# Optimization experiments

Measured on AMD Instinct MI355X. Metric: run time of the kernel, lower is better.

The kernel has to match this reference:

```python
import jax, jax.numpy as jnp
import numpy as np

B, N, D, K = 4, 256, 128, 8
H = 2 * D   # MLP hidden
F3 = 3 * D  # pair feature dim


def setup_inputs() -> dict:
    key = jax.random.key(0)
    ks = jax.random.split(key, 9)
    init = lambda k, shape: (jax.random.normal(k, shape, jnp.float32) * 0.02)
    s = jax.random.normal(ks[0], (B, N, D), jnp.float32)
    return {
        "s": s,
        "Wg1": init(ks[1], (F3, H)), "bg1": jnp.zeros((H,), jnp.float32),
        "Wg2": init(ks[2], (H, 1)),  "bg2": jnp.zeros((1,), jnp.float32),
        "Wa1": init(ks[3], (F3, H)), "ba1": jnp.zeros((H,), jnp.float32),
        "Wa2": init(ks[4], (H, 1)),  "ba2": jnp.zeros((1,), jnp.float32),
    }


def _mlp(x, W1, b1, W2, b2):
    # 2-layer MLP: Linear -> ReLU -> Linear (dropout inactive at eval)
    return jax.nn.relu(x @ W1 + b1) @ W2 + b2


def reference(s, Wg1, bg1, Wg2, bg2, Wa1, ba1, Wa2, ba2):
    b, n, d = s.shape
    si = s[:, :, None, :]                      # [B,N,1,D]
    sj = s[:, None, :, :]                      # [B,1,N,D]
    pair = jnp.concatenate([
        jnp.broadcast_to(si, (b, n, n, d)),
        jnp.broadcast_to(sj, (b, n, n, d)),
        si * sj,
    ], axis=-1)                                # [B,N,N,3D]

    # Stage 1: discrete top-K peer gating
    scores = _mlp(pair, Wg1, bg1, Wg2, bg2)[..., 0]   # [B,N,N]
    k = min(K, n)
    _, topk_idx = jax.lax.top_k(scores, k)            # [B,N,K]
    gate = jax.nn.one_hot(topk_idx, n, dtype=jnp.float32).sum(-2)  # [B,N,N] binary

    # Stage 2: soft relevance weighting over selected peers
    att_logits = _mlp(pair, Wa1, ba1, Wa2, ba2)[..., 0]            # [B,N,N]
    att_logits = jnp.where(gate > 0, att_logits, -jnp.inf)
    att_weights = jnp.nan_to_num(jax.nn.softmax(att_logits, axis=-1))

    ctx = jnp.einsum('bij,bij,bjd->bid', gate, att_weights, s)     # [B,N,D]
    return ctx, gate, att_weights
```

## Files before the change

### kernel.cpp

```cpp
#include <hip/hip_runtime.h>
#include <math.h>

#define B_ 4
#define N_ 256
#define D_ 128
#define H_ 256
#define K_ 8
#define KK 256
#define NJP 64

typedef short v8s __attribute__((ext_vector_type(8)));
typedef float v16f __attribute__((ext_vector_type(16)));

__device__ inline void split_bf16(float x, unsigned short& hi, unsigned short& lo) {
  unsigned u = __float_as_uint(x);
  unsigned uh = u & 0xFFFF0000u;
  hi = (unsigned short)(uh >> 16);
  float r = x - __uint_as_float(uh);
  unsigned ur = __float_as_uint(r);
  ur += 0x7FFFu + ((ur >> 16) & 1u);
  lo = (unsigned short)(ur >> 16);
}

__global__ __launch_bounds__(256) void prep_an(
    const float* __restrict__ s,
    const float* __restrict__ Wg1, const float* __restrict__ bg1,
    const float* __restrict__ Wa1, const float* __restrict__ ba1,
    float* __restrict__ Ag, float* __restrict__ Aa,
    unsigned short* __restrict__ Shi, unsigned short* __restrict__ Slo) {
  const int b = blockIdx.x >> 8;
  const int n = blockIdx.x & 255;
  const int h = threadIdx.x;
  __shared__ float sh[D_];
  if (h < D_) sh[h] = s[(b * N_ + n) * D_ + h];
  __syncthreads();
  float ag = bg1[h], aa = ba1[h];
#pragma unroll 8
  for (int d = 0; d < D_; d++) {
    ag = fmaf(sh[d], Wg1[d * H_ + h], ag);
    aa = fmaf(sh[d], Wa1[d * H_ + h], aa);
  }
  Ag[(b * N_ + n) * H_ + h] = ag;
  Aa[(b * N_ + n) * H_ + h] = aa;
  if (h < D_) {
    unsigned short x, y;
    split_bf16(sh[h], x, y);
    Shi[(b * N_ + n) * D_ + h] = x;
    Slo[(b * N_ + n) * D_ + h] = y;
  }
}

__global__ __launch_bounds__(64) void prep_sw(
    const float* __restrict__ Wg1, const float* __restrict__ Wa1,
    unsigned short* __restrict__ Wghi, unsigned short* __restrict__ Wglo,
    unsigned short* __restrict__ Wahi) {
  const int ks = blockIdx.x >> 3;
  const int tile = blockIdx.x & 7;
  const int lane = threadIdx.x;
  const int h = tile * 32 + (lane & 31);
  const int kbase = ks * 16 + (lane >> 5) * 8;
  const int idx0 = (blockIdx.x * 64 + lane) * 8;
#pragma unroll
  for (int e = 0; e < 8; e++) {
    const int k = kbase + e;
    const int f = (k < D_) ? (2 * D_ + k) : k;
    unsigned short x, y;
    split_bf16(Wg1[f * H_ + h], x, y);
    Wghi[idx0 + e] = x;
    Wglo[idx0 + e] = y;
    unsigned short xa, ya;
    split_bf16(Wa1[f * H_ + h], xa, ya);
    Wahi[idx0 + e] = xa;
  }
}

__global__ __launch_bounds__(256) void prep_sf(
    const unsigned short* __restrict__ Shi, const unsigned short* __restrict__ Slo,
    unsigned short* __restrict__ Sfh, unsigned short* __restrict__ Sfl) {
  const int b = blockIdx.x >> 3, jt = blockIdx.x & 7;
  const int lane = threadIdx.x & 63;
  const int k0 = threadIdx.x >> 6;
  const int j = jt * 32 + (lane & 31);
#pragma unroll
  for (int ksl = k0; ksl < 8; ksl += 4) {
    const int d = ksl * 16 + (lane >> 5) * 8;
    const int src = (b * N_ + j) * D_ + d;
    const int dst = (((b * 8 + jt) * 8 + ksl) * 64 + lane) * 8;
    *(v8s*)(Sfh + dst) = *(const v8s*)(Shi + src);
    *(v8s*)(Sfl + dst) = *(const v8s*)(Slo + src);
  }
}

__device__ inline void arg_better(float v2, int i2, float& v, int& idx) {
  if (v2 > v || (v2 == v && i2 < idx)) { v = v2; idx = i2; }
}

__device__ inline int a_idx(int jl, int k) {
  return (((jl >> 5) * 8 + (k >> 4)) * 64 + ((k >> 3) & 1) * 32 + (jl & 31)) * 8
         + (k & 7);
}
#define ALO 8192

__global__ __launch_bounds__(256, 2) void score_kernel(
    const float* __restrict__ s,
    const float* __restrict__ Ag, const float* __restrict__ Aa,
    const unsigned short* __restrict__ Shi, const unsigned short* __restrict__ Slo,
    const unsigned short* __restrict__ Sfh, const unsigned short* __restrict__ Sfl,
    const unsigned short* __restrict__ Wghi, const unsigned short* __restrict__ Wglo,
    const unsigned short* __restrict__ Wahi,
    const float* __restrict__ Wg2, const float* __restrict__ bg2p,
    const float* __restrict__ Wa2, const float* __restrict__ ba2p,
    float* __restrict__ out) {
  const int b = blockIdx.x >> 8;
  const int i = blockIdx.x & 255;
  const int t = threadIdx.x;
  const int wv = t >> 6, lane = t & 63;
  const int m32 = lane & 31, half32 = lane >> 5;

  __shared__ __align__(16) unsigned short a_all[2 * 8192 + 64];
  __shared__ float si_sh[D_];
  __shared__ float sc_part[8 * NJP];
  __shared__ float scg_sh[N_];
  __shared__ float attl_sh[N_];
  __shared__ float red_v[4];
  __shared__ int red_i[4];
  __shared__ int sel_list[K_];

  if (t < D_) si_sh[t] = s[(b * N_ + i) * D_ + t];

  float agv[2], w2g[2], aav[2], w2a[2];
#pragma unroll
  for (int ht = 0; ht < 2; ht++) {
    const int hg = wv * 64 + ht * 32 + m32;
    agv[ht] = Ag[(b * N_ + i) * H_ + hg];
    w2g[ht] = Wg2[hg];
    aav[ht] = Aa[(b * N_ + i) * H_ + hg];
    w2a[ht] = Wa2[hg];
  }

  const int boff = ((2 * wv) * 64 + lane) * 8;

#pragma unroll 1
  for (int ph = 0; ph < 4; ph++) {
    __syncthreads();
    {
      const int jl = t >> 2, kq = t & 3;
      const int jg = b * N_ + ph * NJP + jl;
      const float* srow = s + jg * D_ + kq * 32;
      const float* sic = si_sh + kq * 32;
#pragma unroll
      for (int u = 0; u < 4; u++) {
        const float4 sv0 = *(const float4*)(srow + u * 8);
        const float4 sv1 = *(const float4*)(srow + u * 8 + 4);
        unsigned short hh[8], ll[8];
        split_bf16(sic[u * 8 + 0] * sv0.x, hh[0], ll[0]);
        split_bf16(sic[u * 8 + 1] * sv0.y, hh[1], ll[1]);
        split_bf16(sic[u * 8 + 2] * sv0.z, hh[2], ll[2]);
        split_bf16(sic[u * 8 + 3] * sv0.w, hh[3], ll[3]);
        split_bf16(sic[u * 8 + 4] * sv1.x, hh[4], ll[4]);
        split_bf16(sic[u * 8 + 5] * sv1.y, hh[5], ll[5]);
        split_bf16(sic[u * 8 + 6] * sv1.z, hh[6], ll[6]);
        split_bf16(sic[u * 8 + 7] * sv1.w, hh[7], ll[7]);
        v8s vh, vl;
#pragma unroll
        for (int e = 0; e < 8; e++) { vh[e] = (short)hh[e]; vl[e] = (short)ll[e]; }
        const int idx = a_idx(jl, kq * 32 + u * 8);
        *(v8s*)(a_all + idx) = vh;
        *(v8s*)(a_all + ALO + idx) = vl;
      }
    }
    __syncthreads();

    const unsigned short* sf_base_h = Sfh + ((b * 8 + ph * 2) * 8) * 512 + lane * 8;
    const unsigned short* sf_base_l = Sfl + ((b * 8 + ph * 2) * 8) * 512 + lane * 8;

    {
      v16f acc[2][2];
#pragma unroll
      for (int jt = 0; jt < 2; jt++)
#pragma unroll
        for (int ht = 0; ht < 2; ht++) acc[jt][ht] = (v16f)(0.f);

      const unsigned short* pgh = Wghi + boff;
      const unsigned short* pgl = Wglo + boff;
      v8s bh[2][2], bl[2][2];
      bh[0][0] = *(const v8s*)pgh;  bh[0][1] = *(const v8s*)(pgh + 512);
      bl[0][0] = *(const v8s*)pgl;  bl[0][1] = *(const v8s*)(pgl + 512);
      pgh += 4096;  pgl += 4096;

      const unsigned short* ahp = a_all + lane * 8;
#pragma unroll 2
      for (int ks = 0; ks < 8; ks++) {
        const int cur = ks & 1, nxt = cur ^ 1;
        bh[nxt][0] = *(const v8s*)pgh;  bh[nxt][1] = *(const v8s*)(pgh + 512);
        bl[nxt][0] = *(const v8s*)pgl;  bl[nxt][1] = *(const v8s*)(pgl + 512);
        pgh += 4096;  pgl += 4096;
        v8s ah0 = *(const v8s*)(ahp);
        v8s ah1 = *(const v8s*)(ahp + 4096);
        v8s al0 = *(const v8s*)(ahp + ALO);
        v8s al1 = *(const v8s*)(ahp + ALO + 4096);
        ahp += 512;
        acc[0][0] = __builtin_amdgcn_mfma_f32_32x32x16_bf16(ah0, bh[cur][0], acc[0][0], 0, 0, 0);
        acc[0][1] = __builtin_amdgcn_mfma_f32_32x32x16_bf16(ah0, bh[cur][1], acc[0][1], 0, 0, 0);
        acc[0][0] = __builtin_amdgcn_mfma_f32_32x32x16_bf16(ah0, bl[cur][0], acc[0][0], 0, 0, 0);
        acc[0][1] = __builtin_amdgcn_mfma_f32_32x32x16_bf16(ah0, bl[cur][1], acc[0][1], 0, 0, 0);
        acc[0][0] = __builtin_amdgcn_mfma_f32_32x32x16_bf16(al0, bh[cur][0], acc[0][0], 0, 0, 0);
        acc[0][1] = __builtin_amdgcn_mfma_f32_32x32x16_bf16(al0, bh[cur][1], acc[0][1], 0, 0, 0);
        acc[1][0] = __builtin_amdgcn_mfma_f32_32x32x16_bf16(ah1, bh[cur][0], acc[1][0], 0, 0, 0);
        acc[1][1] = __builtin_amdgcn_mfma_f32_32x32x16_bf16(ah1, bh[cur][1], acc[1][1], 0, 0, 0);
        acc[1][0] = __builtin_amdgcn_mfma_f32_32x32x16_bf16(ah1, bl[cur][0], acc[1][0], 0, 0, 0);
        acc[1][1] = __builtin_amdgcn_mfma_f32_32x32x16_bf16(ah1, bl[cur][1], acc[1][1], 0, 0, 0);
        acc[1][0] = __builtin_amdgcn_mfma_f32_32x32x16_bf16(al1, bh[cur][0], acc[1][0], 0, 0, 0);
        acc[1][1] = __builtin_amdgcn_mfma_f32_32x32x16_bf16(al1, bh[cur][1], acc[1][1], 0, 0, 0);
      }
      const unsigned short* sfh = sf_base_h;
      const unsigned short* sfl = sf_base_l;
#pragma unroll 2
      for (int ks = 8; ks < 16; ks++) {
        const int cur = ks & 1, nxt = cur ^ 1;
        bh[nxt][0] = *(const v8s*)pgh;  bh[nxt][1] = *(const v8s*)(pgh + 512);
        bl[nxt][0] = *(const v8s*)pgl;  bl[nxt][1] = *(const v8s*)(pgl + 512);
        pgh += 4096;  pgl += 4096;
        v8s ah0 = *(const v8s*)(sfh);
        v8s ah1 = *(const v8s*)(sfh + 4096);
        v8s al0 = *(const v8s*)(sfl);
        v8s al1 = *(const v8s*)(sfl + 4096);
        sfh += 512;  sfl += 512;
        acc[0][0] = __builtin_amdgcn_mfma_f32_32x32x16_bf16(ah0, bh[cur][0], acc[0][0], 0, 0, 0);
        acc[0][1] = __builtin_amdgcn_mfma_f32_32x32x16_bf16(ah0, bh[cur][1], acc[0][1], 0, 0, 0);
        acc[0][0] = __builtin_amdgcn_mfma_f32_32x32x16_bf16(ah0, bl[cur][0], acc[0][0], 0, 0, 0);
        acc[0][1] = __builtin_amdgcn_mfma_f32_32x32x16_bf16(ah0, bl[cur][1], acc[0][1], 0, 0, 0);
        acc[0][0] = __builtin_amdgcn_mfma_f32_32x32x16_bf16(al0, bh[cur][0], acc[0][0], 0, 0, 0);
        acc[0][1] = __builtin_amdgcn_mfma_f32_32x32x16_bf16(al0, bh[cur][1], acc[0][1], 0, 0, 0);
        acc[1][0] = __builtin_amdgcn_mfma_f32_32x32x16_bf16(ah1, bh[cur][0], acc[1][0], 0, 0, 0);
        acc[1][1] = __builtin_amdgcn_mfma_f32_32x32x16_bf16(ah1, bh[cur][1], acc[1][1], 0, 0, 0);
        acc[1][0] = __builtin_amdgcn_mfma_f32_32x32x16_bf16(ah1, bl[cur][0], acc[1][0], 0, 0, 0);
        acc[1][1] = __builtin_amdgcn_mfma_f32_32x32x16_bf16(ah1, bl[cur][1], acc[1][1], 0, 0, 0);
        acc[1][0] = __builtin_amdgcn_mfma_f32_32x32x16_bf16(al1, bh[cur][0], acc[1][0], 0, 0, 0);
        acc[1][1] = __builtin_amdgcn_mfma_f32_32x32x16_bf16(al1, bh[cur][1], acc[1][1], 0, 0, 0);
      }
      float sg[32];
#pragma unroll
      for (int m = 0; m < 32; m++) sg[m] = 0.f;
#pragma unroll
      for (int ht = 0; ht < 2; ht++)
#pragma unroll
        for (int jt = 0; jt < 2; jt++)
#pragma unroll
          for (int r = 0; r < 16; r++) {
            const float z = acc[jt][ht][r] + agv[ht];
            sg[jt * 16 + r] = fmaf(fmaxf(z, 0.f), w2g[ht], sg[jt * 16 + r]);
          }
#pragma unroll
      for (int m = 0; m < 32; m++) {
        float v = sg[m];
#pragma unroll
        for (int off = 1; off <= 16; off <<= 1) v += __shfl_xor(v, off, 64);
        sg[m] = v;
      }
      if (m32 == 0) {
#pragma unroll
        for (int jt = 0; jt < 2; jt++)
#pragma unroll
          for (int r = 0; r < 16; r++) {
            const int jl = jt * 32 + (r & 3) + 8 * (r >> 2) + 4 * half32;
            sc_part[wv * NJP + jl] = sg[jt * 16 + r];
          }
      }
    }

    {
      v16f acc[2][2];
#pragma unroll
      for (int jt = 0; jt < 2; jt++)
#pragma unroll
        for (int ht = 0; ht < 2; ht++) acc[jt][ht] = (v16f)(0.f);

      const unsigned short* pah = Wahi + boff;
      v8s bh[2][2];
      bh[0][0] = *(const v8s*)pah;  bh[0][1] = *(const v8s*)(pah + 512);
      pah += 4096;

      const unsigned short* ahp = a_all + lane * 8;
#pragma unroll 2
      for (int ks = 0; ks < 8; ks++) {
        const int cur = ks & 1, nxt = cur ^ 1;
        bh[nxt][0] = *(const v8s*)pah;  bh[nxt][1] = *(const v8s*)(pah + 512);
        pah += 4096;
        v8s ah0 = *(const v8s*)(ahp);
        v8s ah1 = *(const v8s*)(ahp + 4096);
        ahp += 512;
        acc[0][0] = __builtin_amdgcn_mfma_f32_32x32x16_bf16(ah0, bh[cur][0], acc[0][0], 0, 0, 0);
        acc[0][1] = __builtin_amdgcn_mfma_f32_32x32x16_bf16(ah0, bh[cur][1], acc[0][1], 0, 0, 0);
        acc[1][0] = __builtin_amdgcn_mfma_f32_32x32x16_bf16(ah1, bh[cur][0], acc[1][0], 0, 0, 0);
        acc[1][1] = __builtin_amdgcn_mfma_f32_32x32x16_bf16(ah1, bh[cur][1], acc[1][1], 0, 0, 0);
      }
      const unsigned short* sfh = sf_base_h;
#pragma unroll 2
      for (int ks = 8; ks < 16; ks++) {
        const int cur = ks & 1, nxt = cur ^ 1;
        bh[nxt][0] = *(const v8s*)pah;  bh[nxt][1] = *(const v8s*)(pah + 512);
        pah += 4096;
        v8s ah0 = *(const v8s*)(sfh);
        v8s ah1 = *(const v8s*)(sfh + 4096);
        sfh += 512;
        acc[0][0] = __builtin_amdgcn_mfma_f32_32x32x16_bf16(ah0, bh[cur][0], acc[0][0], 0, 0, 0);
        acc[0][1] = __builtin_amdgcn_mfma_f32_32x32x16_bf16(ah0, bh[cur][1], acc[0][1], 0, 0, 0);
        acc[1][0] = __builtin_amdgcn_mfma_f32_32x32x16_bf16(ah1, bh[cur][0], acc[1][0], 0, 0, 0);
        acc[1][1] = __builtin_amdgcn_mfma_f32_32x32x16_bf16(ah1, bh[cur][1], acc[1][1], 0, 0, 0);
      }
      float sa[32];
#pragma unroll
      for (int m = 0; m < 32; m++) sa[m] = 0.f;
#pragma unroll
      for (int ht = 0; ht < 2; ht++)
#pragma unroll
        for (int jt = 0; jt < 2; jt++)
#pragma unroll
          for (int r = 0; r < 16; r++) {
            const float z = acc[jt][ht][r] + aav[ht];
            sa[jt * 16 + r] = fmaf(fmaxf(z, 0.f), w2a[ht], sa[jt * 16 + r]);
          }
#pragma unroll
      for (int m = 0; m < 32; m++) {
        float v = sa[m];
#pragma unroll
        for (int off = 1; off <= 16; off <<= 1) v += __shfl_xor(v, off, 64);
        sa[m] = v;
      }
      if (m32 == 0) {
#pragma unroll
        for (int jt = 0; jt < 2; jt++)
#pragma unroll
          for (int r = 0; r < 16; r++) {
            const int jl = jt * 32 + (r & 3) + 8 * (r >> 2) + 4 * half32;
            sc_part[4 * NJP + wv * NJP + jl] = sa[jt * 16 + r];
          }
      }
    }
    __syncthreads();
    if (t < NJP) {
      scg_sh[ph * NJP + t] = sc_part[t] + sc_part[NJP + t] + sc_part[2 * NJP + t]
                           + sc_part[3 * NJP + t] + bg2p[0];
      attl_sh[ph * NJP + t] = sc_part[4 * NJP + t] + sc_part[5 * NJP + t]
                            + sc_part[6 * NJP + t] + sc_part[7 * NJP + t] + ba2p[0];
    }
  }
  __syncthreads();

  for (int k = 0; k < K_; k++) {
    float v = scg_sh[t];
    int idx = t;
#pragma unroll
    for (int off = 32; off > 0; off >>= 1) {
      const float vo = __shfl_down(v, off, 64);
      const int io = __shfl_down(idx, off, 64);
      arg_better(vo, io, v, idx);
    }
    if ((t & 63) == 0) { red_v[t >> 6] = v; red_i[t >> 6] = idx; }
    __syncthreads();
    if (t == 0) {
      float bv = red_v[0];
      int bi = red_i[0];
      for (int w = 1; w < 4; w++) arg_better(red_v[w], red_i[w], bv, bi);
      sel_list[k] = bi;
      scg_sh[bi] = -INFINITY;
    }
    __syncthreads();
  }

  bool selj = false;
#pragma unroll
  for (int k = 0; k < K_; k++) selj = selj || (sel_list[k] == t);

  if (t == 0) {
    float m = -INFINITY;
    for (int k = 0; k < K_; k++) m = fmaxf(m, attl_sh[sel_list[k]]);
    float ssum = 0.f;
    for (int k = 0; k < K_; k++) ssum += expf(attl_sh[sel_list[k]] - m);
    red_v[0] = m;
    red_v[1] = ssum;
  }
  __syncthreads();
  const float att = selj ? expf(attl_sh[t] - red_v[0]) / red_v[1] : 0.f;

  float* __restrict__ ctx_out = out;
  float* __restrict__ gate_out = out + B_ * N_ * D_;
  float* __restrict__ att_out = out + B_ * N_ * D_ + B_ * N_ * N_;

  const int row = (b * N_ + i) * N_;
  gate_out[row + t] = selj ? 1.f : 0.f;
  att_out[row + t] = att;

  __syncthreads();
  attl_sh[t] = att;
  __syncthreads();

  if (t < D_) {
    float acc2 = 0.f;
#pragma unroll
    for (int k = 0; k < K_; k++) {
      const int jj = sel_list[k];
      acc2 = fmaf(attl_sh[jj], s[(b * N_ + jj) * D_ + t], acc2);
    }
    ctx_out[(b * N_ + i) * D_ + t] = acc2;
  }
}

extern "C" void kernel_launch(void* const* d_in, const int* in_sizes, int n_in,
                              void* d_out, int out_size, void* d_ws, size_t ws_size,
                              hipStream_t stream) {
  const float* s   = (const float*)d_in[0];
  const float* Wg1 = (const float*)d_in[1];
  const float* bg1 = (const float*)d_in[2];
  const float* Wg2 = (const float*)d_in[3];
  const float* bg2 = (const float*)d_in[4];
  const float* Wa1 = (const float*)d_in[5];
  const float* ba1 = (const float*)d_in[6];
  const float* Wa2 = (const float*)d_in[7];
  const float* ba2 = (const float*)d_in[8];
  float* out = (float*)d_out;

  float* ws = (float*)d_ws;
  float* Ag = ws;
  float* Aa = Ag + B_ * N_ * H_;
  unsigned short* Shi  = (unsigned short*)(Aa + B_ * N_ * H_);
  unsigned short* Slo  = Shi + B_ * N_ * D_;
  unsigned short* Wghi = Slo + B_ * N_ * D_;
  unsigned short* Wglo = Wghi + 65536 + 4096;
  unsigned short* Wahi = Wglo + 65536 + 4096;
  unsigned short* Sfh  = Wahi + 65536 + 4096;
  unsigned short* Sfl  = Sfh + B_ * 32768;

  prep_an<<<dim3(B_ * N_), dim3(256), 0, stream>>>(
      s, Wg1, bg1, Wa1, ba1, Ag, Aa, Shi, Slo);
  prep_sw<<<dim3(128), dim3(64), 0, stream>>>(Wg1, Wa1, Wghi, Wglo, Wahi);
  prep_sf<<<dim3(B_ * 8), dim3(256), 0, stream>>>(Shi, Slo, Sfh, Sfl);
  score_kernel<<<dim3(B_ * N_), dim3(256), 0, stream>>>(
      s, Ag, Aa, Shi, Slo, Sfh, Sfl, Wghi, Wglo, Wahi, Wg2, bg2, Wa2, ba2, out);
}
```

Measured before the change: 264.5 us.

## Merge prep kernels into one launch and fuse gate/attention MFMA loops

Combines the three preprocessing kernels into a single launch that branches on block index, and builds the fragment-layout split of s directly from fp32, which drops the intermediate Shi/Slo buffers. In the score kernel, the gating and attention first-layer GEMMs now share one loop, so the A fragments (LDS tile and Sf global loads) are read once and feed both weight sets. This cuts launch overhead and duplicate operand traffic, but holds eight accumulators live at once, which raises register pressure and may hurt occupancy under the 2-blocks launch bound.

```diff
diff --git a/kernel.cpp b/kernel.cpp
--- a/kernel.cpp
+++ b/kernel.cpp
@@ -6,7 +6,6 @@
 #define D_ 128
 #define H_ 256
 #define K_ 8
-#define KK 256
 #define NJP 64
 
 typedef short v8s __attribute__((ext_vector_type(8)));
@@ -22,72 +21,73 @@
   lo = (unsigned short)(ur >> 16);
 }
 
-__global__ __launch_bounds__(256) void prep_an(
+__global__ __launch_bounds__(256) void prep_all(
     const float* __restrict__ s,
     const float* __restrict__ Wg1, const float* __restrict__ bg1,
     const float* __restrict__ Wa1, const float* __restrict__ ba1,
     float* __restrict__ Ag, float* __restrict__ Aa,
-    unsigned short* __restrict__ Shi, unsigned short* __restrict__ Slo) {
-  const int b = blockIdx.x >> 8;
-  const int n = blockIdx.x & 255;
-  const int h = threadIdx.x;
+    unsigned short* __restrict__ Wghi, unsigned short* __restrict__ Wglo,
+    unsigned short* __restrict__ Wahi,
+    unsigned short* __restrict__ Sfh, unsigned short* __restrict__ Sfl) {
   __shared__ float sh[D_];
-  if (h < D_) sh[h] = s[(b * N_ + n) * D_ + h];
-  __syncthreads();
-  float ag = bg1[h], aa = ba1[h];
+  const int blk = blockIdx.x;
+  if (blk < 1024) {
+    const int b = blk >> 8, n = blk & 255, h = threadIdx.x;
+    if (h < D_) sh[h] = s[(b * N_ + n) * D_ + h];
+    __syncthreads();
+    float ag = bg1[h], aa = ba1[h];
 #pragma unroll 8
-  for (int d = 0; d < D_; d++) {
-    ag = fmaf(sh[d], Wg1[d * H_ + h], ag);
-    aa = fmaf(sh[d], Wa1[d * H_ + h], aa);
-  }
-  Ag[(b * N_ + n) * H_ + h] = ag;
-  Aa[(b * N_ + n) * H_ + h] = aa;
-  if (h < D_) {
-    unsigned short x, y;
-    split_bf16(sh[h], x, y);
-    Shi[(b * N_ + n) * D_ + h] = x;
-    Slo[(b * N_ + n) * D_ + h] = y;
-  }
-}
-
-__global__ __launch_bounds__(64) void prep_sw(
-    const float* __restrict__ Wg1, const float* __restrict__ Wa1,
-    unsigned short* __restrict__ Wghi, unsigned short* __restrict__ Wglo,
-    unsigned short* __restrict__ Wahi) {
-  const int ks = blockIdx.x >> 3;
-  const int tile = blockIdx.x & 7;
-  const int lane = threadIdx.x;
-  const int h = tile * 32 + (lane & 31);
-  const int kbase = ks * 16 + (lane >> 5) * 8;
-  const int idx0 = (blockIdx.x * 64 + lane) * 8;
-#pragma unroll
-  for (int e = 0; e < 8; e++) {
-    const int k = kbase + e;
-    const int f = (k < D_) ? (2 * D_ + k) : k;
-    unsigned short x, y;
-    split_bf16(Wg1[f * H_ + h], x, y);
-    Wghi[idx0 + e] = x;
-    Wglo[idx0 + e] = y;
-    unsigned short xa, ya;
-    split_bf16(Wa1[f * H_ + h], xa, ya);
-    Wahi[idx0 + e] = xa;
-  }
-}
-
-__global__ __launch_bounds__(256) void prep_sf(
-    const unsigned short* __restrict__ Shi, const unsigned short* __restrict__ Slo,
-    unsigned short* __restrict__ Sfh, unsigned short* __restrict__ Sfl) {
-  const int b = blockIdx.x >> 3, jt = blockIdx.x & 7;
-  const int lane = threadIdx.x & 63;
-  const int k0 = threadIdx.x >> 6;
-  const int j = jt * 32 + (lane & 31);
-#pragma unroll
-  for (int ksl = k0; ksl < 8; ksl += 4) {
-    const int d = ksl * 16 + (lane >> 5) * 8;
-    const int src = (b * N_ + j) * D_ + d;
-    const int dst = (((b * 8 + jt) * 8 + ksl) * 64 + lane) * 8;
-    *(v8s*)(Sfh + dst) = *(const v8s*)(Shi + src);
-    *(v8s*)(Sfl + dst) = *(const v8s*)(Slo + src);
+    for (int d = 0; d < D_; d++) {
+      ag = fmaf(sh[d], Wg1[d * H_ + h], ag);
+      aa = fmaf(sh[d], Wa1[d * H_ + h], aa);
+    }
+    Ag[(b * N_ + n) * H_ + h] = ag;
+    Aa[(b * N_ + n) * H_ + h] = aa;
+  } else if (blk < 1152) {
+    const int id = blk - 1024;
+    if (threadIdx.x < 64) {
+      const int ks = id >> 3, tile = id & 7, lane = threadIdx.x;
+      const int h = tile * 32 + (lane & 31);
+      const int kbase = ks * 16 + (lane >> 5) * 8;
+      const int idx0 = (id * 64 + lane) * 8;
+#pragma unroll
+      for (int e = 0; e < 8; e++) {
+        const int k = kbase + e;
+        const int f = (k < D_) ? (2 * D_ + k) : k;
+        unsigned short x, y;
+        split_bf16(Wg1[f * H_ + h], x, y);
+        Wghi[idx0 + e] = x;
+        Wglo[idx0 + e] = y;
+        unsigned short xa, ya;
+        split_bf16(Wa1[f * H_ + h], xa, ya);
+        Wahi[idx0 + e] = xa;
+      }
+    }
+  } else {
+    const int id = blk - 1152;
+    const int b = id >> 3, jt = id & 7;
+    const int lane = threadIdx.x & 63, k0 = threadIdx.x >> 6;
+    const int j = jt * 32 + (lane & 31);
+#pragma unroll
+    for (int ksl = k0; ksl < 8; ksl += 4) {
+      const int d = ksl * 16 + (lane >> 5) * 8;
+      const float* sp = s + (b * N_ + j) * D_ + d;
+      const float4 f0 = *(const float4*)(sp);
+      const float4 f1 = *(const float4*)(sp + 4);
+      v8s vh, vl;
+      unsigned short x, y;
+      split_bf16(f0.x, x, y); vh[0] = (short)x; vl[0] = (short)y;
+      split_bf16(f0.y, x, y); vh[1] = (short)x; vl[1] = (short)y;
+      split_bf16(f0.z, x, y); vh[2] = (short)x; vl[2] = (short)y;
+      split_bf16(f0.w, x, y); vh[3] = (short)x; vl[3] = (short)y;
+      split_bf16(f1.x, x, y); vh[4] = (short)x; vl[4] = (short)y;
+      split_bf16(f1.y, x, y); vh[5] = (short)x; vl[5] = (short)y;
+      split_bf16(f1.z, x, y); vh[6] = (short)x; vl[6] = (short)y;
+      split_bf16(f1.w, x, y); vh[7] = (short)x; vl[7] = (short)y;
+      const int dst = (((b * 8 + jt) * 8 + ksl) * 64 + lane) * 8;
+      *(v8s*)(Sfh + dst) = vh;
+      *(v8s*)(Sfl + dst) = vl;
+    }
   }
 }
 
@@ -104,7 +104,6 @@
 __global__ __launch_bounds__(256, 2) void score_kernel(
     const float* __restrict__ s,
     const float* __restrict__ Ag, const float* __restrict__ Aa,
-    const unsigned short* __restrict__ Shi, const unsigned short* __restrict__ Slo,
     const unsigned short* __restrict__ Sfh, const unsigned short* __restrict__ Sfl,
     const unsigned short* __restrict__ Wghi, const unsigned short* __restrict__ Wglo,
     const unsigned short* __restrict__ Wahi,
@@ -117,7 +116,7 @@
   const int wv = t >> 6, lane = t & 63;
   const int m32 = lane & 31, half32 = lane >> 5;
 
-  __shared__ __align__(16) unsigned short a_all[2 * 8192 + 64];
+  __shared__ __align__(16) unsigned short a_all[2 * ALO + 64];
   __shared__ float si_sh[D_];
   __shared__ float sc_part[8 * NJP];
   __shared__ float scg_sh[N_];
@@ -140,6 +139,8 @@
 
   const int boff = ((2 * wv) * 64 + lane) * 8;
 
+#define MF(A_, B_v, C_) C_ = __builtin_amdgcn_mfma_f32_32x32x16_bf16(A_, B_v, C_, 0, 0, 0)
+
 #pragma unroll 1
   for (int ph = 0; ph < 4; ph++) {
     __syncthreads();
@@ -152,18 +153,16 @@
       for (int u = 0; u < 4; u++) {
         const float4 sv0 = *(const float4*)(srow + u * 8);
         const float4 sv1 = *(const float4*)(srow + u * 8 + 4);
-        unsigned short hh[8], ll[8];
-        split_bf16(sic[u * 8 + 0] * sv0.x, hh[0], ll[0]);
-        split_bf16(sic[u * 8 + 1] * sv0.y, hh[1], ll[1]);
-        split_bf16(sic[u * 8 + 2] * sv0.z, hh[2], ll[2]);
-        split_bf16(sic[u * 8 + 3] * sv0.w, hh[3], ll[3]);
-        split_bf16(sic[u * 8 + 4] * sv1.x, hh[4], ll[4]);
-        split_bf16(sic[u * 8 + 5] * sv1.y, hh[5], ll[5]);
-        split_bf16(sic[u * 8 + 6] * sv1.z, hh[6], ll[6]);
-        split_bf16(sic[u * 8 + 7] * sv1.w, hh[7], ll[7]);
         v8s vh, vl;
-#pragma unroll
-        for (int e = 0; e < 8; e++) { vh[e] = (short)hh[e]; vl[e] = (short)ll[e]; }
+        unsigned short x, y;
+        split_bf16(sic[u * 8 + 0] * sv0.x, x, y); vh[0] = (short)x; vl[0] = (short)y;
+        split_bf16(sic[u * 8 + 1] * sv0.y, x, y); vh[1] = (short)x; vl[1] = (short)y;
+        split_bf16(sic[u * 8 + 2] * sv0.z, x, y); vh[2] = (short)x; vl[2] = (short)y;
+        split_bf16(sic[u * 8 + 3] * sv0.w, x, y); vh[3] = (short)x; vl[3] = (short)y;
+        split_bf16(sic[u * 8 + 4] * sv1.x, x, y); vh[4] = (short)x; vl[4] = (short)y;
+        split_bf16(sic[u * 8 + 5] * sv1.y, x, y); vh[5] = (short)x; vl[5] = (short)y;
+        split_bf16(sic[u * 8 + 6] * sv1.z, x, y); vh[6] = (short)x; vl[6] = (short)y;
+        split_bf16(sic[u * 8 + 7] * sv1.w, x, y); vh[7] = (short)x; vl[7] = (short)y;
         const int idx = a_idx(jl, kq * 32 + u * 8);
         *(v8s*)(a_all + idx) = vh;
         *(v8s*)(a_all + ALO + idx) = vl;
@@ -174,19 +173,19 @@
     const unsigned short* sf_base_h = Sfh + ((b * 8 + ph * 2) * 8) * 512 + lane * 8;
     const unsigned short* sf_base_l = Sfl + ((b * 8 + ph * 2) * 8) * 512 + lane * 8;
 
+    v16f g00, g01, g10, g11, a00, a01, a10, a11;
+    g00 = g01 = g10 = g11 = (v16f)(0.f);
+    a00 = a01 = a10 = a11 = (v16f)(0.f);
+
     {
-      v16f acc[2][2];
-#pragma unroll
-      for (int jt = 0; jt < 2; jt++)
-#pragma unroll
-        for (int ht = 0; ht < 2; ht++) acc[jt][ht] = (v16f)(0.f);
-
       const unsigned short* pgh = Wghi + boff;
       const unsigned short* pgl = Wglo + boff;
-      v8s bh[2][2], bl[2][2];
+      const unsigned short* pah = Wahi + boff;
+      v8s bh[2][2], bl[2][2], ba[2][2];
       bh[0][0] = *(const v8s*)pgh;  bh[0][1] = *(const v8s*)(pgh + 512);
       bl[0][0] = *(const v8s*)pgl;  bl[0][1] = *(const v8s*)(pgl + 512);
-      pgh += 4096;  pgl += 4096;
+      ba[0][0] = *(const v8s*)pah;  ba[0][1] = *(const v8s*)(pah + 512);
+      pgh += 4096;  pgl += 4096;  pah += 4096;
 
       const unsigned short* ahp = a_all + lane * 8;
 #pragma unroll 2
@@ -194,24 +193,21 @@
         const int cur = ks & 1, nxt = cur ^ 1;
         bh[nxt][0] = *(const v8s*)pgh;  bh[nxt][1] = *(const v8s*)(pgh + 512);
         bl[nxt][0] = *(const v8s*)pgl;  bl[nxt][1] = *(const v8s*)(pgl + 512);
-        pgh += 4096;  pgl += 4096;
+        ba[nxt][0] = *(const v8s*)pah;  ba[nxt][1] = *(const v8s*)(pah + 512);
+        pgh += 4096;  pgl += 4096;  pah += 4096;
         v8s ah0 = *(const v8s*)(ahp);
         v8s ah1 = *(const v8s*)(ahp + 4096);
         v8s al0 = *(const v8s*)(ahp + ALO);
         v8s al1 = *(const v8s*)(ahp + ALO + 4096);
         ahp += 512;
-        acc[0][0] = __builtin_amdgcn_mfma_f32_32x32x16_bf16(ah0, bh[cur][0], acc[0][0], 0, 0, 0);
-        acc[0][1] = __builtin_amdgcn_mfma_f32_32x32x16_bf16(ah0, bh[cur][1], acc[0][1], 0, 0, 0);
-        acc[0][0] = __builtin_amdgcn_mfma_f32_32x32x16_bf16(ah0, bl[cur][0], acc[0][0], 0, 0, 0);
-        acc[0][1] = __builtin_amdgcn_mfma_f32_32x32x16_bf16(ah0, bl[cur][1], acc[0][1], 0, 0, 0);
-        acc[0][0] = __builtin_amdgcn_mfma_f32_32x32x16_bf16(al0, bh[cur][0], acc[0][0], 0, 0, 0);
-        acc[0][1] = __builtin_amdgcn_mfma_f32_32x32x16_bf16(al0, bh[cur][1], acc[0][1], 0, 0, 0);
-        acc[1][0] = __builtin_amdgcn_mfma_f32_32x32x16_bf16(ah1, bh[cur][0], acc[1][0], 0, 0, 0);
-        acc[1][1] = __builtin_amdgcn_mfma_f32_32x32x16_bf16(ah1, bh[cur][1], acc[1][1], 0, 0, 0);
-        acc[1][0] = __builtin_amdgcn_mfma_f32_32x32x16_bf16(ah1, bl[cur][0], acc[1][0], 0, 0, 0);
-        acc[1][1] = __builtin_amdgcn_mfma_f32_32x32x16_bf16(ah1, bl[cur][1], acc[1][1], 0, 0, 0);
-        acc[1][0] = __builtin_amdgcn_mfma_f32_32x32x16_bf16(al1, bh[cur][0], acc[1][0], 0, 0, 0);
-        acc[1][1] = __builtin_amdgcn_mfma_f32_32x32x16_bf16(al1, bh[cur][1], acc[1][1], 0, 0, 0);
+        MF(ah0, bh[cur][0], g00); MF(ah0, bh[cur][1], g01);
+        MF(ah0, ba[cur][0], a00); MF(ah0, ba[cur][1], a01);
+        MF(ah0, bl[cur][0], g00); MF(ah0, bl[cur][1], g01);
+        MF(al0, bh[cur][0], g00); MF(al0, bh[cur][1], g01);
+        MF(ah1, bh[cur][0], g10); MF(ah1, bh[cur][1], g11);
+        MF(ah1, ba[cur][0], a10); MF(ah1, ba[cur][1], a11);
+        MF(ah1, bl[cur][0], g10); MF(ah1, bl[cur][1], g11);
+        MF(al1, bh[cur][0], g10); MF(al1, bh[cur][1], g11);
       }
       const unsigned short* sfh = sf_base_h;
       const unsigned short* sfl = sf_base_l;
@@ -220,37 +216,35 @@
         const int cur = ks & 1, nxt = cur ^ 1;
         bh[nxt][0] = *(const v8s*)pgh;  bh[nxt][1] = *(const v8s*)(pgh + 512);
         bl[nxt][0] = *(const v8s*)pgl;  bl[nxt][1] = *(const v8s*)(pgl + 512);
-        pgh += 4096;  pgl += 4096;
+        ba[nxt][0] = *(const v8s*)pah;  ba[nxt][1] = *(const v8s*)(pah + 512);
+        pgh += 4096;  pgl += 4096;  pah += 4096;
         v8s ah0 = *(const v8s*)(sfh);
         v8s ah1 = *(const v8s*)(sfh + 4096);
         v8s al0 = *(const v8s*)(sfl);
         v8s al1 = *(const v8s*)(sfl + 4096);
         sfh += 512;  sfl += 512;
-        acc[0][0] = __builtin_amdgcn_mfma_f32_32x32x16_bf16(ah0, bh[cur][0], acc[0][0], 0, 0, 0);
-        acc[0][1] = __builtin_amdgcn_mfma_f32_32x32x16_bf16(ah0, bh[cur][1], acc[0][1], 0, 0, 0);
-        acc[0][0] = __builtin_amdgcn_mfma_f32_32x32x16_bf16(ah0, bl[cur][0], acc[0][0], 0, 0, 0);
-        acc[0][1] = __builtin_amdgcn_mfma_f32_32x32x16_bf16(ah0, bl[cur][1], acc[0][1], 0, 0, 0);
-        acc[0][0] = __builtin_amdgcn_mfma_f32_32x32x16_bf16(al0, bh[cur][0], acc[0][0], 0, 0, 0);
-        acc[0][1] = __builtin_amdgcn_mfma_f32_32x32x16_bf16(al0, bh[cur][1], acc[0][1], 0, 0, 0);
-        acc[1][0] = __builtin_amdgcn_mfma_f32_32x32x16_bf16(ah1, bh[cur][0], acc[1][0], 0, 0, 0);
-        acc[1][1] = __builtin_amdgcn_mfma_f32_32x32x16_bf16(ah1, bh[cur][1], acc[1][1], 0, 0, 0);
-        acc[1][0] = __builtin_amdgcn_mfma_f32_32x32x16_bf16(ah1, bl[cur][0], acc[1][0], 0, 0, 0);
-        acc[1][1] = __builtin_amdgcn_mfma_f32_32x32x16_bf16(ah1, bl[cur][1], acc[1][1], 0, 0, 0);
-        acc[1][0] = __builtin_amdgcn_mfma_f32_32x32x16_bf16(al1, bh[cur][0], acc[1][0], 0, 0, 0);
-        acc[1][1] = __builtin_amdgcn_mfma_f32_32x32x16_bf16(al1, bh[cur][1], acc[1][1], 0, 0, 0);
-      }
+        MF(ah0, bh[cur][0], g00); MF(ah0, bh[cur][1], g01);
+        MF(ah0, ba[cur][0], a00); MF(ah0, ba[cur][1], a01);
+        MF(ah0, bl[cur][0], g00); MF(ah0, bl[cur][1], g01);
+        MF(al0, bh[cur][0], g00); MF(al0, bh[cur][1], g01);
+        MF(ah1, bh[cur][0], g10); MF(ah1, bh[cur][1], g11);
+        MF(ah1, ba[cur][0], a10); MF(ah1, ba[cur][1], a11);
+        MF(ah1, bl[cur][0], g10); MF(ah1, bl[cur][1], g11);
+        MF(al1, bh[cur][0], g10); MF(al1, bh[cur][1], g11);
+      }
+    }
+
+    {
       float sg[32];
 #pragma unroll
       for (int m = 0; m < 32; m++) sg[m] = 0.f;
 #pragma unroll
-      for (int ht = 0; ht < 2; ht++)
-#pragma unroll
-        for (int jt = 0; jt < 2; jt++)
-#pragma unroll
-          for (int r = 0; r < 16; r++) {
-            const float z = acc[jt][ht][r] + agv[ht];
-            sg[jt * 16 + r] = fmaf(fmaxf(z, 0.f), w2g[ht], sg[jt * 16 + r]);
-          }
+      for (int r = 0; r < 16; r++) {
+        sg[r]      = fmaf(fmaxf(g00[r] + agv[0], 0.f), w2g[0], sg[r]);
+        sg[r]      = fmaf(fmaxf(g01[r] + agv[1], 0.f), w2g[1], sg[r]);
+        sg[16 + r] = fmaf(fmaxf(g10[r] + agv[0], 0.f), w2g[0], sg[16 + r]);
+        sg[16 + r] = fmaf(fmaxf(g11[r] + agv[1], 0.f), w2g[1], sg[16 + r]);
+      }
 #pragma unroll
       for (int m = 0; m < 32; m++) {
         float v = sg[m];
@@ -267,60 +261,16 @@
             sc_part[wv * NJP + jl] = sg[jt * 16 + r];
           }
       }
-    }
-
-    {
-      v16f acc[2][2];
-#pragma unroll
-      for (int jt = 0; jt < 2; jt++)
-#pragma unroll
-        for (int ht = 0; ht < 2; ht++) acc[jt][ht] = (v16f)(0.f);
-
-      const unsigned short* pah = Wahi + boff;
-      v8s bh[2][2];
-      bh[0][0] = *(const v8s*)pah;  bh[0][1] = *(const v8s*)(pah + 512);
-      pah += 4096;
-
-      const unsigned short* ahp = a_all + lane * 8;
-#pragma unroll 2
-      for (int ks = 0; ks < 8; ks++) {
-        const int cur = ks & 1, nxt = cur ^ 1;
-        bh[nxt][0] = *(const v8s*)pah;  bh[nxt][1] = *(const v8s*)(pah + 512);
-        pah += 4096;
-        v8s ah0 = *(const v8s*)(ahp);
-        v8s ah1 = *(const v8s*)(ahp + 4096);
-        ahp += 512;
-        acc[0][0] = __builtin_amdgcn_mfma_f32_32x32x16_bf16(ah0, bh[cur][0], acc[0][0], 0, 0, 0);
-        acc[0][1] = __builtin_amdgcn_mfma_f32_32x32x16_bf16(ah0, bh[cur][1], acc[0][1], 0, 0, 0);
-        acc[1][0] = __builtin_amdgcn_mfma_f32_32x32x16_bf16(ah1, bh[cur][0], acc[1][0], 0, 0, 0);
-        acc[1][1] = __builtin_amdgcn_mfma_f32_32x32x16_bf16(ah1, bh[cur][1], acc[1][1], 0, 0, 0);
-      }
-      const unsigned short* sfh = sf_base_h;
-#pragma unroll 2
-      for (int ks = 8; ks < 16; ks++) {
-        const int cur = ks & 1, nxt = cur ^ 1;
-        bh[nxt][0] = *(const v8s*)pah;  bh[nxt][1] = *(const v8s*)(pah + 512);
-        pah += 4096;
-        v8s ah0 = *(const v8s*)(sfh);
-        v8s ah1 = *(const v8s*)(sfh + 4096);
-        sfh += 512;
-        acc[0][0] = __builtin_amdgcn_mfma_f32_32x32x16_bf16(ah0, bh[cur][0], acc[0][0], 0, 0, 0);
-        acc[0][1] = __builtin_amdgcn_mfma_f32_32x32x16_bf16(ah0, bh[cur][1], acc[0][1], 0, 0, 0);
-        acc[1][0] = __builtin_amdgcn_mfma_f32_32x32x16_bf16(ah1, bh[cur][0], acc[1][0], 0, 0, 0);
-        acc[1][1] = __builtin_amdgcn_mfma_f32_32x32x16_bf16(ah1, bh[cur][1], acc[1][1], 0, 0, 0);
-      }
       float sa[32];
 #pragma unroll
       for (int m = 0; m < 32; m++) sa[m] = 0.f;
 #pragma unroll
-      for (int ht = 0; ht < 2; ht++)
-#pragma unroll
-        for (int jt = 0; jt < 2; jt++)
-#pragma unroll
-          for (int r = 0; r < 16; r++) {
-            const float z = acc[jt][ht][r] + aav[ht];
-            sa[jt * 16 + r] = fmaf(fmaxf(z, 0.f), w2a[ht], sa[jt * 16 + r]);
-          }
+      for (int r = 0; r < 16; r++) {
+        sa[r]      = fmaf(fmaxf(a00[r] + aav[0], 0.f), w2a[0], sa[r]);
+        sa[r]      = fmaf(fmaxf(a01[r] + aav[1], 0.f), w2a[1], sa[r]);
+        sa[16 + r] = fmaf(fmaxf(a10[r] + aav[0], 0.f), w2a[0], sa[16 + r]);
+        sa[16 + r] = fmaf(fmaxf(a11[r] + aav[1], 0.f), w2a[1], sa[16 + r]);
+      }
 #pragma unroll
       for (int m = 0; m < 32; m++) {
         float v = sa[m];
@@ -405,6 +355,7 @@
     }
     ctx_out[(b * N_ + i) * D_ + t] = acc2;
   }
+#undef MF
 }
 
 extern "C" void kernel_launch(void* const* d_in, const int* in_sizes, int n_in,
@@ -424,18 +375,14 @@
   float* ws = (float*)d_ws;
   float* Ag = ws;
   float* Aa = Ag + B_ * N_ * H_;
-  unsigned short* Shi  = (unsigned short*)(Aa + B_ * N_ * H_);
-  unsigned short* Slo  = Shi + B_ * N_ * D_;
-  unsigned short* Wghi = Slo + B_ * N_ * D_;
+  unsigned short* Wghi = (unsigned short*)(Aa + B_ * N_ * H_);
   unsigned short* Wglo = Wghi + 65536 + 4096;
   unsigned short* Wahi = Wglo + 65536 + 4096;
   unsigned short* Sfh  = Wahi + 65536 + 4096;
   unsigned short* Sfl  = Sfh + B_ * 32768;
 
-  prep_an<<<dim3(B_ * N_), dim3(256), 0, stream>>>(
-      s, Wg1, bg1, Wa1, ba1, Ag, Aa, Shi, Slo);
-  prep_sw<<<dim3(128), dim3(64), 0, stream>>>(Wg1, Wa1, Wghi, Wglo, Wahi);
-  prep_sf<<<dim3(B_ * 8), dim3(256), 0, stream>>>(Shi, Slo, Sfh, Sfl);
+  prep_all<<<dim3(1184), dim3(256), 0, stream>>>(
+      s, Wg1, bg1, Wa1, ba1, Ag, Aa, Wghi, Wglo, Wahi, Sfh, Sfl);
   score_kernel<<<dim3(B_ * N_), dim3(256), 0, stream>>>(
-      s, Ag, Aa, Shi, Slo, Sfh, Sfl, Wghi, Wglo, Wahi, Wg2, bg2, Wa2, ba2, out);
-}
+      s, Ag, Aa, Sfh, Sfl, Wghi, Wglo, Wahi, Wg2, bg2, Wa2, ba2, out);
+}
```

After: 241.4 us. 1.1x faster.
